# Performance work log

Hardware: AMD Instinct MI355X
Metric: run time of the kernel (lower is better)

The kernel has to match this reference:

```python
import jax, jax.numpy as jnp
import numpy as np

DIM = 192
HEADS = 6
WIN = 7


def conv2d(x, w, b, pad):
    # x: (N,C,H,W), w: (O,I,kh,kw)
    y = jax.lax.conv_general_dilated(
        x, w, window_strides=(1, 1), padding=[(pad, pad), (pad, pad)],
        dimension_numbers=('NCHW', 'OIHW', 'NCHW'))
    return y + b[None, :, None, None]


def setup_inputs() -> dict:
    key = jax.random.key(0)
    ks = jax.random.split(key, 4)
    B, C, H, W = 8, DIM, 128, 128
    D = C // HEADS
    s = lambda fan_in: 1.0 / np.sqrt(fan_in)
    return {
        'x': jax.random.normal(ks[0], (B, C, H, W), jnp.float32),
        'w_qkv': jax.random.normal(ks[1], (3 * C, C, 1, 1), jnp.float32) * s(C),
        'b_qkv': jnp.zeros((3 * C,), jnp.float32),
        'w_attn': jax.random.normal(ks[2], (WIN * WIN, 2 * D, WIN, WIN), jnp.float32) * s(2 * D * WIN * WIN),
        'b_attn': jnp.zeros((WIN * WIN,), jnp.float32),
        'w_proj': jax.random.normal(ks[3], (C, C, 1, 1), jnp.float32) * s(C),
        'b_proj': jnp.zeros((C,), jnp.float32),
    }


def reference(x, w_qkv, b_qkv, w_attn, b_attn, w_proj, b_proj):
    B, C, H, W = x.shape
    D = C // HEADS
    scale = D ** -0.5
    # qkv 1x1 conv -> (B, 3, heads, D, H, W)
    qkv = conv2d(x, w_qkv, b_qkv, 0).reshape(B, 3, HEADS, D, H, W)
    q, v = qkv[:, 0], qkv[:, 2]  # NOTE: original code uses q twice (not k)
    q_flat = q.reshape(B * HEADS, D, H, W)
    qq = jnp.concatenate([q_flat * scale, q_flat], axis=1)  # (B*heads, 2D, H, W)
    # conv-generated local attention logits over winSize^2 positions
    attn = conv2d(qq, w_attn, b_attn, WIN // 2)
    attn = jax.nn.softmax(attn, axis=1).reshape(B, HEADS, WIN * WIN, H, W)
    # sum over window dim of v (broadcast over k) * attn (broadcast over d)
    out = jnp.einsum('bhkxy,bhdxy->bhdxy', attn, v).reshape(B, C, H, W)
    return conv2d(out, w_proj, b_proj, 0)
```

## Files before the change

kernel.cpp:

```cpp
#include <hip/hip_runtime.h>
#include <stdint.h>
#include <stddef.h>


#define CDIM 192
#define HWPX 16384

typedef __attribute__((ext_vector_type(8))) short short8;
typedef __attribute__((ext_vector_type(4))) float floatx4;

__device__ __forceinline__ unsigned short f2bf(float f) {
    union { float f; unsigned int u; } v; v.f = f;
    return (unsigned short)((v.u + 0x7FFFu + ((v.u >> 16) & 1u)) >> 16);
}

__global__ __launch_bounds__(192) void prep_kernel(
    const float* __restrict__ w_qkv, const float* __restrict__ b_qkv,
    const float* __restrict__ w_proj, const float* __restrict__ b_proj,
    unsigned short* __restrict__ Mb, float* __restrict__ bias)
{
    const int o = blockIdx.x, c = threadIdx.x;
    const float* wpr = w_proj + o * CDIM;
    const float* wv  = w_qkv + 2 * CDIM * CDIM;
    float a0 = 0.f, a1 = 0.f, a2 = 0.f, a3 = 0.f;
    #pragma unroll 12
    for (int k = 0; k < CDIM; k += 4) {
        a0 = fmaf(wpr[k + 0], wv[(k + 0) * CDIM + c], a0);
        a1 = fmaf(wpr[k + 1], wv[(k + 1) * CDIM + c], a1);
        a2 = fmaf(wpr[k + 2], wv[(k + 2) * CDIM + c], a2);
        a3 = fmaf(wpr[k + 3], wv[(k + 3) * CDIM + c], a3);
    }
    Mb[o * CDIM + c] = f2bf((a0 + a1) + (a2 + a3));

    __shared__ float red[CDIM];
    red[c] = wpr[c] * b_qkv[2 * CDIM + c];
    __syncthreads();
    if (c < 64) {
        float v = red[c] + red[c + 64] + red[c + 128];
        #pragma unroll
        for (int off = 32; off > 0; off >>= 1) v += __shfl_down(v, off);
        if (c == 0) bias[o] = v + b_proj[o];
    }
}

__global__ __launch_bounds__(512, 4) void fused_kernel(
    const float* __restrict__ x,
    const unsigned short* __restrict__ Mb,
    const float* __restrict__ bias,
    float* __restrict__ out)
{
    __shared__ short8 Xl[24 * 64];

    const int tid  = threadIdx.x;
    const int bid  = blockIdx.x;
    const int b    = bid >> 8;
    const int p0   = (bid & 255) << 6;

    const int lane = tid & 63;
    const int wv8  = tid >> 6;
    const int n    = lane & 15;
    const int q    = lane >> 4;

    const float* xb = x + (size_t)b * CDIM * HWPX + p0;
    #pragma unroll
    for (int i = 0; i < 3; ++i) {
        const int f  = i * 8 + wv8;
        const int pt = f / 6, ks = f % 6;
        const float* src = xb + (size_t)(ks * 32 + q * 8) * HWPX + (pt * 16 + n);
        float v[8];
        #pragma unroll
        for (int j = 0; j < 8; ++j) v[j] = src[(size_t)j * HWPX];
        short8 fr;
        #pragma unroll
        for (int j = 0; j < 8; ++j) fr[j] = (short)f2bf(v[j]);
        Xl[f * 64 + lane] = fr;
    }
    __syncthreads();

    const int w2 = wv8 & 3;
    const int wp = wv8 >> 2;

    short8 a[3][6];
    #pragma unroll
    for (int t = 0; t < 3; ++t) {
        const unsigned short* ab = Mb + (size_t)((w2 * 3 + t) * 16 + n) * CDIM + q * 8;
        #pragma unroll
        for (int ks = 0; ks < 6; ++ks)
            a[t][ks] = *(const short8*)(ab + ks * 32);
    }

    floatx4 acc[3][2];
    #pragma unroll
    for (int t = 0; t < 3; ++t)
        #pragma unroll
        for (int ph = 0; ph < 2; ++ph)
            acc[t][ph] = (floatx4){0.f, 0.f, 0.f, 0.f};

    #pragma unroll
    for (int ph = 0; ph < 2; ++ph) {
        const int pt = wp * 2 + ph;
        #pragma unroll
        for (int ks = 0; ks < 6; ++ks) {
            short8 bf = Xl[(pt * 6 + ks) * 64 + lane];
            #pragma unroll
            for (int t = 0; t < 3; ++t)
                acc[t][ph] = __builtin_amdgcn_mfma_f32_16x16x32_bf16(
                    a[t][ks], bf, acc[t][ph], 0, 0, 0);
        }
    }

    float* ob = out + (size_t)b * CDIM * HWPX + p0;
    #pragma unroll
    for (int t = 0; t < 3; ++t) {
        #pragma unroll
        for (int r = 0; r < 4; ++r) {
            const int o = (w2 * 3 + t) * 16 + q * 4 + r;
            const float bo = bias[o];
            float* orow = ob + (size_t)o * HWPX + n;
            #pragma unroll
            for (int ph = 0; ph < 2; ++ph)
                orow[(wp * 2 + ph) * 16] = acc[t][ph][r] + bo;
        }
    }
}

extern "C" void kernel_launch(void* const* d_in, const int* in_sizes, int n_in,
                              void* d_out, int out_size, void* d_ws, size_t ws_size,
                              hipStream_t stream) {
    const float* x      = (const float*)d_in[0];
    const float* w_qkv  = (const float*)d_in[1];
    const float* b_qkv  = (const float*)d_in[2];
    const float* w_proj = (const float*)d_in[5];
    const float* b_proj = (const float*)d_in[6];
    float* out = (float*)d_out;

    unsigned short* Mb = (unsigned short*)d_ws;
    float* bias = (float*)((char*)d_ws + CDIM * CDIM * sizeof(unsigned short));

    const int B = in_sizes[0] / (CDIM * HWPX);

    prep_kernel<<<CDIM, CDIM, 0, stream>>>(w_qkv, b_qkv, w_proj, b_proj, Mb, bias);
    fused_kernel<<<B * 256, 512, 0, stream>>>(x, Mb, bias, out);
}
```

Measured before the change: 219.7 us.

## Vectorize x staging and output stores by swapping MFMA operand roles

```diff
diff --git a/kernel.cpp b/kernel.cpp
--- a/kernel.cpp
+++ b/kernel.cpp
@@ -5,13 +5,17 @@
 
 #define CDIM 192
 #define HWPX 16384
+#define SROW 68
 
 typedef __attribute__((ext_vector_type(8))) short short8;
 typedef __attribute__((ext_vector_type(4))) float floatx4;
 
-__device__ __forceinline__ unsigned short f2bf(float f) {
+__device__ __forceinline__ unsigned int f2bf_u(float f) {
     union { float f; unsigned int u; } v; v.f = f;
-    return (unsigned short)((v.u + 0x7FFFu + ((v.u >> 16) & 1u)) >> 16);
+    return (v.u + 0x7FFFu + ((v.u >> 16) & 1u)) >> 16;
+}
+__device__ __forceinline__ unsigned int pack2(float lo, float hi) {
+    return f2bf_u(lo) | (f2bf_u(hi) << 16);
 }
 
 __global__ __launch_bounds__(192) void prep_kernel(
@@ -30,7 +34,7 @@
         a2 = fmaf(wpr[k + 2], wv[(k + 2) * CDIM + c], a2);
         a3 = fmaf(wpr[k + 3], wv[(k + 3) * CDIM + c], a3);
     }
-    Mb[o * CDIM + c] = f2bf((a0 + a1) + (a2 + a3));
+    Mb[o * CDIM + c] = (unsigned short)f2bf_u((a0 + a1) + (a2 + a3));
 
     __shared__ float red[CDIM];
     red[c] = wpr[c] * b_qkv[2 * CDIM + c];
@@ -43,13 +47,13 @@
     }
 }
 
-__global__ __launch_bounds__(512, 4) void fused_kernel(
+__global__ __launch_bounds__(256, 3) void fused_kernel(
     const float* __restrict__ x,
     const unsigned short* __restrict__ Mb,
     const float* __restrict__ bias,
     float* __restrict__ out)
 {
-    __shared__ short8 Xl[24 * 64];
+    __shared__ unsigned int Xw[96 * SROW];
 
     const int tid  = threadIdx.x;
     const int bid  = blockIdx.x;
@@ -57,69 +61,67 @@
     const int p0   = (bid & 255) << 6;
 
     const int lane = tid & 63;
-    const int wv8  = tid >> 6;
+    const int w    = tid >> 6;
     const int n    = lane & 15;
     const int q    = lane >> 4;
 
     const float* xb = x + (size_t)b * CDIM * HWPX + p0;
     #pragma unroll
-    for (int i = 0; i < 3; ++i) {
-        const int f  = i * 8 + wv8;
-        const int pt = f / 6, ks = f % 6;
-        const float* src = xb + (size_t)(ks * 32 + q * 8) * HWPX + (pt * 16 + n);
-        float v[8];
-        #pragma unroll
-        for (int j = 0; j < 8; ++j) v[j] = src[(size_t)j * HWPX];
-        short8 fr;
-        #pragma unroll
-        for (int j = 0; j < 8; ++j) fr[j] = (short)f2bf(v[j]);
-        Xl[f * 64 + lane] = fr;
+    for (int it = 0; it < 6; ++it) {
+        const int g = it * 256 + tid;
+        const int r = g >> 4, a = g & 15;
+        const float* s0 = xb + (size_t)(2 * r) * HWPX + 4 * a;
+        floatx4 fe = *(const floatx4*)s0;
+        floatx4 fo = *(const floatx4*)(s0 + HWPX);
+        uint4 wd;
+        wd.x = pack2(fe[0], fo[0]);
+        wd.y = pack2(fe[1], fo[1]);
+        wd.z = pack2(fe[2], fo[2]);
+        wd.w = pack2(fe[3], fo[3]);
+        *(uint4*)&Xw[r * SROW + 4 * a] = wd;
     }
     __syncthreads();
 
-    const int w2 = wv8 & 3;
-    const int wp = wv8 >> 2;
-
-    short8 a[3][6];
-    #pragma unroll
-    for (int t = 0; t < 3; ++t) {
-        const unsigned short* ab = Mb + (size_t)((w2 * 3 + t) * 16 + n) * CDIM + q * 8;
-        #pragma unroll
-        for (int ks = 0; ks < 6; ++ks)
-            a[t][ks] = *(const short8*)(ab + ks * 32);
-    }
-
-    floatx4 acc[3][2];
+    floatx4 acc[3][4];
     #pragma unroll
     for (int t = 0; t < 3; ++t)
         #pragma unroll
-        for (int ph = 0; ph < 2; ++ph)
-            acc[t][ph] = (floatx4){0.f, 0.f, 0.f, 0.f};
+        for (int pt = 0; pt < 4; ++pt)
+            acc[t][pt] = (floatx4){0.f, 0.f, 0.f, 0.f};
 
     #pragma unroll
-    for (int ph = 0; ph < 2; ++ph) {
-        const int pt = wp * 2 + ph;
+    for (int ks = 0; ks < 6; ++ks) {
+        short8 mf[3];
         #pragma unroll
-        for (int ks = 0; ks < 6; ++ks) {
-            short8 bf = Xl[(pt * 6 + ks) * 64 + lane];
+        for (int t = 0; t < 3; ++t)
+            mf[t] = *(const short8*)(Mb + (size_t)((w * 3 + t) * 16 + n) * CDIM
+                                     + ks * 32 + q * 8);
+        #pragma unroll
+        for (int pt = 0; pt < 4; ++pt) {
+            union { unsigned int u[4]; short8 s; } A;
+            const int base = (ks * 16 + q * 4) * SROW + pt * 16 + n;
+            A.u[0] = Xw[base];
+            A.u[1] = Xw[base + SROW];
+            A.u[2] = Xw[base + 2 * SROW];
+            A.u[3] = Xw[base + 3 * SROW];
             #pragma unroll
             for (int t = 0; t < 3; ++t)
-                acc[t][ph] = __builtin_amdgcn_mfma_f32_16x16x32_bf16(
-                    a[t][ks], bf, acc[t][ph], 0, 0, 0);
+                acc[t][pt] = __builtin_amdgcn_mfma_f32_16x16x32_bf16(
+                    A.s, mf[t], acc[t][pt], 0, 0, 0);
         }
     }
 
     float* ob = out + (size_t)b * CDIM * HWPX + p0;
     #pragma unroll
     for (int t = 0; t < 3; ++t) {
+        const int o = (w * 3 + t) * 16 + n;
+        const float bo = bias[o];
+        float* orow = ob + (size_t)o * HWPX + q * 4;
         #pragma unroll
-        for (int r = 0; r < 4; ++r) {
-            const int o = (w2 * 3 + t) * 16 + q * 4 + r;
-            const float bo = bias[o];
-            float* orow = ob + (size_t)o * HWPX + n;
-            #pragma unroll
-            for (int ph = 0; ph < 2; ++ph)
-                orow[(wp * 2 + ph) * 16] = acc[t][ph][r] + bo;
+        for (int pt = 0; pt < 4; ++pt) {
+            floatx4 v = acc[t][pt];
+            v[0] += bo; v[1] += bo; v[2] += bo; v[3] += bo;
+            *(floatx4*)(orow + pt * 16) = v;
         }
     }
 }
@@ -140,5 +142,5 @@
     const int B = in_sizes[0] / (CDIM * HWPX);
 
     prep_kernel<<<CDIM, CDIM, 0, stream>>>(w_qkv, b_qkv, w_proj, b_proj, Mb, bias);
-    fused_kernel<<<B * 256, 512, 0, stream>>>(x, Mb, bias, out);
+    fused_kernel<<<B * 256, 256, 0, stream>>>(x, Mb, bias, out);
 }
```

New measurement: 209.4 us. 1.05x faster.
